# Performance work log

Hardware: AMD Instinct MI355X
Metric: run time of the kernel (lower is better)

The kernel has to match this reference:

```python
import jax, jax.numpy as jnp
import numpy as np

BN_EPS = 1e-5


def setup_inputs() -> dict:
    key = jax.random.key(0)
    ks = jax.random.split(key, 8)
    B, C, H, W = 8, 256, 64, 64
    Cqk = C // 8  # query/key channels = out_channels // 8
    x = jax.random.normal(ks[0], (B, C, H, W), dtype=jnp.float32)
    # 1x1 convs == per-pixel matmuls; kaiming-normal-ish scale
    wq = jax.random.normal(ks[1], (Cqk, C), dtype=jnp.float32) * np.sqrt(2.0 / C)
    bq = jnp.zeros((Cqk,), dtype=jnp.float32)
    wk = jax.random.normal(ks[2], (Cqk, C), dtype=jnp.float32) * np.sqrt(2.0 / C)
    bk = jnp.zeros((Cqk,), dtype=jnp.float32)
    wv = jax.random.normal(ks[3], (C, C), dtype=jnp.float32) * np.sqrt(2.0 / C)
    bv = jnp.zeros((C,), dtype=jnp.float32)
    # gamma is initialized to 0 in the original; use a small nonzero value so
    # the attention path actually contributes (and has nontrivial gradients)
    gamma = jnp.full((1,), 0.5, dtype=jnp.float32)
    bn_weight = jnp.ones((C,), dtype=jnp.float32)
    bn_bias = jnp.zeros((C,), dtype=jnp.float32)
    return {"x": x, "wq": wq, "bq": bq, "wk": wk, "bk": bk,
            "wv": wv, "bv": bv, "gamma": gamma,
            "bn_weight": bn_weight, "bn_bias": bn_bias}


def reference(x, wq, bq, wk, bk, wv, bv, gamma, bn_weight, bn_bias):
    B, C, H, W = x.shape
    N = H * W
    xf = x.reshape(B, C, N)  # (B, C, N)
    # 1x1 conv projections as channel matmuls
    q = jnp.einsum('oc,bcn->bno', wq, xf) + bq            # (B, N, Cqk)
    k = jnp.einsum('oc,bcn->bon', wk, xf) + bk[:, None]   # (B, Cqk, N)
    v = jnp.einsum('oc,bcn->bon', wv, xf) + bv[:, None]   # (B, C, N)
    # attention[b, i, j] = softmax_j(q_i . k_j)  -- full N x N matrix
    scores = jnp.einsum('bno,bom->bnm', q, k)             # (B, N, N)
    attn = jax.nn.softmax(scores, axis=2)
    # out[b, c, i] = sum_j v[b, c, j] * attn[b, i, j]
    out = jnp.einsum('bcj,bij->bci', v, attn)             # (B, C, N)
    out = out.reshape(B, C, H, W)
    out = gamma[0] * out + x
    # BatchNorm2d in training mode: batch statistics over (B, H, W)
    mean = jnp.mean(out, axis=(0, 2, 3), keepdims=True)
    var = jnp.var(out, axis=(0, 2, 3), keepdims=True)
    out = (out - mean) * jax.lax.rsqrt(var + BN_EPS)
    out = out * bn_weight[None, :, None, None] + bn_bias[None, :, None, None]
    return jax.nn.relu(out)
```

## Files before the change

### kernel.cpp

```cpp
#include <hip/hip_runtime.h>
#include <stdint.h>

#define B_ 8
#define C_ 256
#define N_ 4096
#define CQK 32
#define VPANEL (C_ * 64)

typedef __attribute__((ext_vector_type(8))) _Float16 f16x8;
typedef __attribute__((ext_vector_type(4))) float f32x4;

__device__ __forceinline__ unsigned short f2bf_rne(float f) {
  unsigned u = __builtin_bit_cast(unsigned, f);
  u += 0x7FFFu + ((u >> 16) & 1u);
  return (unsigned short)(u >> 16);
}

__global__ __launch_bounds__(256) void xpose_kernel(
    const float* __restrict__ x, _Float16* __restrict__ xT)
{
  __shared__ float xs[64 * 129];
  const int t  = threadIdx.x;
  const int blk = blockIdx.x;
  const int nt = blk & 31;
  const int ct = (blk >> 5) & 3;
  const int b  = blk >> 7;
  const int c0 = ct * 64, n0 = nt * 128;

  #pragma unroll
  for (int p = 0; p < 8; ++p) {
    int cc = p * 8 + (t >> 5);
    int nn = (t & 31) * 4;
    float4 v = *(const float4*)(x + ((size_t)(b * C_ + c0 + cc)) * N_ + n0 + nn);
    xs[cc * 129 + nn]     = v.x;
    xs[cc * 129 + nn + 1] = v.y;
    xs[cc * 129 + nn + 2] = v.z;
    xs[cc * 129 + nn + 3] = v.w;
  }
  __syncthreads();
  #pragma unroll
  for (int p = 0; p < 4; ++p) {
    int id = p * 256 + t;
    int cchunk = id & 7, n = id >> 3;
    _Float16 h[8];
    #pragma unroll
    for (int j = 0; j < 8; ++j) h[j] = (_Float16)xs[(cchunk * 8 + j) * 129 + n];
    *(f16x8*)(xT + ((size_t)(b * N_) + n0 + n) * C_ + c0 + cchunk * 8) = *(f16x8*)h;
  }
}

__global__ __launch_bounds__(256) void wconv_kernel(
    const float* __restrict__ wq, const float* __restrict__ wk,
    const float* __restrict__ wv, _Float16* __restrict__ wf)
{
  int idx = blockIdx.x * 256 + threadIdx.x;
  int e = idx * 4;
  int o = e >> 8, c = e & 255;
  const float* src;
  if (o < 32)      src = wq + o * 256 + c;
  else if (o < 64) src = wk + (o - 32) * 256 + c;
  else             src = wv + (o - 64) * 256 + c;
  float4 v = *(const float4*)src;
  _Float16 h[4] = {(_Float16)v.x, (_Float16)v.y, (_Float16)v.z, (_Float16)v.w};
  *(uint2*)(wf + e) = *(uint2*)h;
}

__global__ __launch_bounds__(256, 4) void proj_gemm_kernel(
    const _Float16* __restrict__ xT, const _Float16* __restrict__ wf,
    const float* __restrict__ bq, const float* __restrict__ bk,
    const float* __restrict__ bv,
    _Float16* __restrict__ qf, _Float16* __restrict__ kf,
    _Float16* __restrict__ vout)
{
  const int t = threadIdx.x, lane = t & 63;
  const int w = t >> 6;
  const int l15 = lane & 15, q4 = lane >> 4;
  const int blk = blockIdx.x;
  const int otile = blk % 5;
  const int nt = blk / 5;
  const int b  = nt >> 5;
  const int n0 = (nt & 31) * 128;
  const int o0w = (w & 1) * 32;
  const int n0w = (w >> 1) * 64;

  f32x4 acc[2][4];
  const f32x4 zf = {0.f, 0.f, 0.f, 0.f};
  #pragma unroll
  for (int a = 0; a < 2; ++a)
    #pragma unroll
    for (int bb = 0; bb < 4; ++bb) acc[a][bb] = zf;

  const _Float16* wbase = wf + (size_t)(otile * 64 + o0w) * 256;
  const _Float16* xbase = xT + ((size_t)(b * N_) + n0 + n0w) * C_;

  #pragma unroll
  for (int kc = 0; kc < 8; ++kc) {
    f16x8 af[2], bfr[4];
    #pragma unroll
    for (int ob = 0; ob < 2; ++ob)
      af[ob] = *(const f16x8*)(wbase + (ob * 16 + l15) * 256 + kc * 32 + q4 * 8);
    #pragma unroll
    for (int nb = 0; nb < 4; ++nb)
      bfr[nb] = *(const f16x8*)(xbase + (nb * 16 + l15) * 256 + kc * 32 + q4 * 8);
    #pragma unroll
    for (int ob = 0; ob < 2; ++ob)
      #pragma unroll
      for (int nb = 0; nb < 4; ++nb)
        acc[ob][nb] = __builtin_amdgcn_mfma_f32_16x16x32_f16(af[ob], bfr[nb], acc[ob][nb], 0, 0, 0);
  }

  if (otile == 0) {
    _Float16* dst = (o0w == 0) ? qf : kf;
    const float* bias = (o0w == 0) ? bq : bk;
    const float qsc = (o0w == 0) ? 1.4426950408889634f : 1.0f;
    #pragma unroll
    for (int ob = 0; ob < 2; ++ob) {
      float4 b4 = *(const float4*)(bias + ob * 16 + q4 * 4);
      #pragma unroll
      for (int nb = 0; nb < 4; ++nb) {
        int pixel = n0 + n0w + nb * 16 + l15;
        _Float16 h[4];
        h[0] = (_Float16)((acc[ob][nb][0] + b4.x) * qsc);
        h[1] = (_Float16)((acc[ob][nb][1] + b4.y) * qsc);
        h[2] = (_Float16)((acc[ob][nb][2] + b4.z) * qsc);
        h[3] = (_Float16)((acc[ob][nb][3] + b4.w) * qsc);
        *(uint2*)(dst + ((size_t)(b * N_) + pixel) * CQK + ob * 16 + q4 * 4) = *(uint2*)h;
      }
    }
  } else {
    int cbase = (otile - 1) * 64 + o0w;
    const int panel = (n0 + n0w) >> 6;
    _Float16* vpan = vout + ((size_t)(b * 64 + panel)) * VPANEL;
    #pragma unroll
    for (int ob = 0; ob < 2; ++ob) {
      float4 b4 = *(const float4*)(bv + cbase + ob * 16 + q4 * 4);
      #pragma unroll
      for (int nb = 0; nb < 4; ++nb) {
        int jj = nb * 16 + l15;
        #pragma unroll
        for (int r = 0; r < 4; ++r) {
          int c = cbase + ob * 16 + q4 * 4 + r;
          float bval = (r == 0) ? b4.x : (r == 1) ? b4.y : (r == 2) ? b4.z : b4.w;
          vpan[(size_t)c * 64 + jj] = (_Float16)(acc[ob][nb][r] + bval);
        }
      }
    }
  }
}

#define ATTN_BODY(K, BUF) do { \
   \
  f16x8 kx_[8]; \
  { const _Float16* kp_ = kbase + (size_t)(K) * 128 * CQK; \
    _Pragma("unroll") \
    for (int jb = 0; jb < 8; ++jb) kx_[jb] = *(const f16x8*)(kp_ + jb * 16 * CQK); } \
   \
  f16x8 vx_[16]; \
  { const _Float16* vp_ = vbase + (size_t)(K) * 2 * VPANEL; \
    _Pragma("unroll") \
    for (int ks = 0; ks < 4; ++ks) \
      _Pragma("unroll") \
      for (int cb = 0; cb < 4; ++cb) \
        vx_[ks * 4 + cb] = *(const f16x8*)(vp_ + (ks >> 1) * VPANEL + cb * 1024 + (ks & 1) * 32); } \
   \
  f32x4 sv_[8]; \
  _Pragma("unroll") \
  for (int jb = 0; jb < 8; ++jb) \
    sv_[jb] = __builtin_amdgcn_mfma_f32_16x16x32_f16(kx_[jb], qfr, zf, 0, 0, 0); \
  float lm_ = sv_[0][0]; \
  _Pragma("unroll") \
  for (int jb = 0; jb < 8; ++jb) \
    lm_ = fmaxf(lm_, fmaxf(fmaxf(sv_[jb][0], sv_[jb][1]), fmaxf(sv_[jb][2], sv_[jb][3]))); \
  lm_ = fmaxf(lm_, __shfl_xor(lm_, 16)); \
  lm_ = fmaxf(lm_, __shfl_xor(lm_, 32)); \
  bool upd_ = lm_ > mold + 8.0f; \
  unsigned long long bal_ = __ballot(upd_);      \
  float alpha_ = upd_ ? exp2f(mold - lm_) : 1.0f; \
  if (upd_) mold = lm_; \
  float ts_ = 0.f; \
  { char* pb_ = (char*)Plds + (BUF) * 17408 + (w * 16 + l15) * 272 + q4 * 8; \
    _Pragma("unroll") \
    for (int jb = 0; jb < 8; ++jb) { \
      float p0_ = exp2f(sv_[jb][0] - mold), p1_ = exp2f(sv_[jb][1] - mold); \
      float p2_ = exp2f(sv_[jb][2] - mold), p3_ = exp2f(sv_[jb][3] - mold); \
      ts_ += (p0_ + p1_) + (p2_ + p3_); \
      _Float16 h_[4] = {(_Float16)p0_, (_Float16)p1_, (_Float16)p2_, (_Float16)p3_}; \
      *(uint2*)(pb_ + jb * 32) = *(uint2*)h_; } } \
  if (q4 == 0) alphal[(BUF) * 64 + w * 16 + l15] = alpha_; \
  if (lane == 0) flagw[(BUF) * 4 + w] = (bal_ != 0ull) ? 1 : 0; \
  ts_ += __shfl_xor(ts_, 16); \
  ts_ += __shfl_xor(ts_, 32); \
  lrun = lrun * alpha_ + ts_; \
  asm volatile("s_waitcnt lgkmcnt(0)" ::: "memory"); \
  __builtin_amdgcn_sched_barrier(0); \
  __builtin_amdgcn_s_barrier(); \
  asm volatile("" ::: "memory"); \
   \
  { int4 fl_ = *(const int4*)(flagw + (BUF) * 4); \
    if (fl_.x | fl_.y | fl_.z | fl_.w) { \
      _Pragma("unroll") \
      for (int ib = 0; ib < 4; ++ib) { \
        float av_ = alphal[(BUF) * 64 + ib * 16 + l15]; \
        _Pragma("unroll") \
        for (int cb = 0; cb < 4; ++cb) \
          _Pragma("unroll") \
          for (int r = 0; r < 4; ++r) acc[cb][ib][r] *= av_; } } } \
   \
  __builtin_amdgcn_s_setprio(1); \
  _Pragma("unroll") \
  for (int ks = 0; ks < 4; ++ks) { \
    f16x8 pf_[4]; \
    _Pragma("unroll") \
    for (int ib = 0; ib < 4; ++ib) \
      pf_[ib] = *(const f16x8*)((char*)Plds + (BUF) * 17408 + (ib * 16 + l15) * 272 + ks * 64 + q4 * 16); \
    _Pragma("unroll") \
    for (int cb = 0; cb < 4; ++cb) \
      _Pragma("unroll") \
      for (int ib = 0; ib < 4; ++ib) \
        acc[cb][ib] = __builtin_amdgcn_mfma_f32_16x16x32_f16(vx_[ks * 4 + cb], pf_[ib], acc[cb][ib], 0, 0, 0); \
  } \
  __builtin_amdgcn_s_setprio(0); \
} while (0)

__global__ __launch_bounds__(256, 2) void attn_kernel(
    const float* __restrict__ x, const float* __restrict__ gptr,
    const _Float16* __restrict__ qf, const _Float16* __restrict__ kf,
    const _Float16* __restrict__ vf, unsigned short* __restrict__ yout)
{
  __shared__ __align__(16) char smem[35648];
  _Float16* Plds  = (_Float16*)smem;
  float* alphal = (float*)(smem + 34816);
  int*   flagw  = (int*)(smem + 35328);
  float* lrowl  = (float*)(smem + 35360);

  const int t = threadIdx.x, lane = t & 63;
  const int w = t >> 6;
  const int l15 = lane & 15, q4 = lane >> 4;
  const int b  = blockIdx.x & 7;
  const int it = blockIdx.x >> 3;
  const int i0 = it * 64;
  const float gamma = gptr[0];

  const f16x8 qfr = *(const f16x8*)(qf + ((size_t)(b * N_) + i0 + w * 16 + l15) * CQK + q4 * 8);

  const _Float16* kbase = kf + ((size_t)(b * N_) + l15) * CQK + q4 * 8;
  const _Float16* vbase = vf + (size_t)b * (64 * VPANEL)
                             + ((size_t)(w * 64 + l15)) * 64 + q4 * 8;

  f32x4 acc[4][4];
  const f32x4 zf = {0.f, 0.f, 0.f, 0.f};
  #pragma unroll
  for (int a = 0; a < 4; ++a)
    #pragma unroll
    for (int bb = 0; bb < 4; ++bb) acc[a][bb] = zf;

  float mold = -1e30f, lrun = 0.f;

  #pragma unroll 1
  for (int k = 0; k < 32; k += 2) {
    ATTN_BODY(k, 0);
    ATTN_BODY(k + 1, 1);
  }

  if (q4 == 0) lrowl[w * 16 + l15] = lrun;
  __syncthreads();
  #pragma unroll
  for (int ib = 0; ib < 4; ++ib) {
    float linv = 1.0f / lrowl[ib * 16 + l15];
    int i = i0 + ib * 16 + l15;
    #pragma unroll
    for (int cb = 0; cb < 4; ++cb) {
      #pragma unroll
      for (int r = 0; r < 4; ++r) {
        int c = w * 64 + cb * 16 + q4 * 4 + r;
        size_t off = ((size_t)(b * C_) + c) * N_ + i;
        float o = acc[cb][ib][r] * linv;
        yout[off] = f2bf_rne(fmaf(gamma, o, x[off]));
      }
    }
  }
}

__global__ __launch_bounds__(256) void bnstats_kernel(
    const unsigned short* __restrict__ y, float* __restrict__ meanw, float* __restrict__ rstdw)
{
  const int c = blockIdx.x;
  const int t = threadIdx.x;
  float s1 = 0.f, s2 = 0.f;
  for (int b = 0; b < B_; ++b) {
    const unsigned short* p = y + ((size_t)(b * C_ + c)) * N_;
    #pragma unroll
    for (int r = 0; r < 2; ++r) {
      uint4 u = *(const uint4*)(p + r * 2048 + t * 8);
      unsigned uu[4] = {u.x, u.y, u.z, u.w};
      #pragma unroll
      for (int k = 0; k < 4; ++k) {
        float a = __builtin_bit_cast(float, uu[k] << 16);
        float bb = __builtin_bit_cast(float, uu[k] & 0xFFFF0000u);
        s1 += a + bb;
        s2 += a * a + bb * bb;
      }
    }
  }
  __shared__ float r1[256], r2[256];
  r1[t] = s1; r2[t] = s2;
  __syncthreads();
  for (int s = 128; s > 0; s >>= 1) {
    if (t < s) { r1[t] += r1[t + s]; r2[t] += r2[t + s]; }
    __syncthreads();
  }
  if (t == 0) {
    float mean = r1[0] * (1.0f / 32768.0f);
    float var  = r2[0] * (1.0f / 32768.0f) - mean * mean;
    meanw[c] = mean;
    rstdw[c] = rsqrtf(var + 1e-5f);
  }
}

__global__ __launch_bounds__(256) void bnapply_kernel(
    const unsigned short* __restrict__ y, float* __restrict__ out,
    const float* __restrict__ meanw, const float* __restrict__ rstdw,
    const float* __restrict__ bnw, const float* __restrict__ bnb)
{
  size_t idx = (size_t)blockIdx.x * 256 + threadIdx.x;
  size_t el = idx * 8;
  int c = (int)((el >> 12) & 255);
  float sc = bnw[c] * rstdw[c];
  float sh = fmaf(-meanw[c], sc, bnb[c]);
  uint4 u = *(const uint4*)(y + el);
  unsigned uu[4] = {u.x, u.y, u.z, u.w};
  float4 o0, o1;
  float v[8];
  #pragma unroll
  for (int k = 0; k < 4; ++k) {
    v[2 * k]     = __builtin_bit_cast(float, uu[k] << 16);
    v[2 * k + 1] = __builtin_bit_cast(float, uu[k] & 0xFFFF0000u);
  }
  o0.x = fmaxf(fmaf(v[0], sc, sh), 0.f);
  o0.y = fmaxf(fmaf(v[1], sc, sh), 0.f);
  o0.z = fmaxf(fmaf(v[2], sc, sh), 0.f);
  o0.w = fmaxf(fmaf(v[3], sc, sh), 0.f);
  o1.x = fmaxf(fmaf(v[4], sc, sh), 0.f);
  o1.y = fmaxf(fmaf(v[5], sc, sh), 0.f);
  o1.z = fmaxf(fmaf(v[6], sc, sh), 0.f);
  o1.w = fmaxf(fmaf(v[7], sc, sh), 0.f);
  *(float4*)(out + el) = o0;
  *(float4*)(out + el + 4) = o1;
}

extern "C" void kernel_launch(void* const* d_in, const int* in_sizes, int n_in,
                              void* d_out, int out_size, void* d_ws, size_t ws_size,
                              hipStream_t stream)
{
  const float* x   = (const float*)d_in[0];
  const float* wq  = (const float*)d_in[1];
  const float* bq  = (const float*)d_in[2];
  const float* wk  = (const float*)d_in[3];
  const float* bk  = (const float*)d_in[4];
  const float* wv  = (const float*)d_in[5];
  const float* bv  = (const float*)d_in[6];
  const float* gm  = (const float*)d_in[7];
  const float* bnw = (const float*)d_in[8];
  const float* bnb = (const float*)d_in[9];
  float* out = (float*)d_out;

  _Float16* xT  = (_Float16*)d_out;
  _Float16* vfp = (_Float16*)((char*)d_out + (size_t)B_ * C_ * N_ * 2);

  char* ws = (char*)d_ws;
  _Float16* qf = (_Float16*)(ws);
  _Float16* kf = (_Float16*)(ws + ((size_t)2 << 20));
  unsigned short* yout = (unsigned short*)(ws + ((size_t)4 << 20));
  _Float16* wf = (_Float16*)(ws + ((size_t)21 << 20));
  float* meanw = (float*)(ws + ((size_t)22 << 20));
  float* rstdw = (float*)(ws + ((size_t)22 << 20) + 4096);

  hipLaunchKernelGGL(xpose_kernel, dim3(1024), dim3(256), 0, stream, x, xT);
  hipLaunchKernelGGL(wconv_kernel, dim3(80), dim3(256), 0, stream, wq, wk, wv, wf);
  hipLaunchKernelGGL(proj_gemm_kernel, dim3(1280), dim3(256), 0, stream,
                     xT, wf, bq, bk, bv, qf, kf, vfp);
  hipLaunchKernelGGL(attn_kernel, dim3(512), dim3(256), 0, stream,
                     x, gm, qf, kf, vfp, yout);
  hipLaunchKernelGGL(bnstats_kernel, dim3(256), dim3(256), 0, stream,
                     yout, meanw, rstdw);
  hipLaunchKernelGGL(bnapply_kernel, dim3(4096), dim3(256), 0, stream,
                     yout, out, meanw, rstdw, bnw, bnb);
}
```

Measured before the change: 297.8 us.

## Fuse x transpose/fp16 conversion into projection GEMM via shared memory

Removes the separate transpose kernel that wrote an fp16 transposed copy of x to global memory. Each projection block now loads a 64-pixel tile of x in fp32, transposes and converts it into an LDS panel, then loops over all five output tiles (q/k plus four v tiles) reusing that panel. This avoids a global write and re-read of the transposed activations and one launch, at the cost of fewer blocks (512), lower occupancy from larger LDS use, and a serialized loop over output tiles per block.

New measurement: 288.9 us. 3.0% less time.

```diff
diff --git a/kernel.cpp b/kernel.cpp
--- a/kernel.cpp
+++ b/kernel.cpp
@@ -14,39 +14,6 @@
   unsigned u = __builtin_bit_cast(unsigned, f);
   u += 0x7FFFu + ((u >> 16) & 1u);
   return (unsigned short)(u >> 16);
-}
-
-__global__ __launch_bounds__(256) void xpose_kernel(
-    const float* __restrict__ x, _Float16* __restrict__ xT)
-{
-  __shared__ float xs[64 * 129];
-  const int t  = threadIdx.x;
-  const int blk = blockIdx.x;
-  const int nt = blk & 31;
-  const int ct = (blk >> 5) & 3;
-  const int b  = blk >> 7;
-  const int c0 = ct * 64, n0 = nt * 128;
-
-  #pragma unroll
-  for (int p = 0; p < 8; ++p) {
-    int cc = p * 8 + (t >> 5);
-    int nn = (t & 31) * 4;
-    float4 v = *(const float4*)(x + ((size_t)(b * C_ + c0 + cc)) * N_ + n0 + nn);
-    xs[cc * 129 + nn]     = v.x;
-    xs[cc * 129 + nn + 1] = v.y;
-    xs[cc * 129 + nn + 2] = v.z;
-    xs[cc * 129 + nn + 3] = v.w;
-  }
-  __syncthreads();
-  #pragma unroll
-  for (int p = 0; p < 4; ++p) {
-    int id = p * 256 + t;
-    int cchunk = id & 7, n = id >> 3;
-    _Float16 h[8];
-    #pragma unroll
-    for (int j = 0; j < 8; ++j) h[j] = (_Float16)xs[(cchunk * 8 + j) * 129 + n];
-    *(f16x8*)(xT + ((size_t)(b * N_) + n0 + n) * C_ + c0 + cchunk * 8) = *(f16x8*)h;
-  }
 }
 
 __global__ __launch_bounds__(256) void wconv_kernel(
@@ -65,96 +32,120 @@
   *(uint2*)(wf + e) = *(uint2*)h;
 }
 
-__global__ __launch_bounds__(256, 4) void proj_gemm_kernel(
-    const _Float16* __restrict__ xT, const _Float16* __restrict__ wf,
+__global__ __launch_bounds__(256, 2) void proj_fused_kernel(
+    const float* __restrict__ x, const _Float16* __restrict__ wf,
     const float* __restrict__ bq, const float* __restrict__ bk,
     const float* __restrict__ bv,
     _Float16* __restrict__ qf, _Float16* __restrict__ kf,
     _Float16* __restrict__ vout)
 {
+  __shared__ float xs[64 * 65];
+  __shared__ _Float16 bp[32 * 64 * 8];
+
   const int t = threadIdx.x, lane = t & 63;
   const int w = t >> 6;
   const int l15 = lane & 15, q4 = lane >> 4;
   const int blk = blockIdx.x;
-  const int otile = blk % 5;
-  const int nt = blk / 5;
-  const int b  = nt >> 5;
-  const int n0 = (nt & 31) * 128;
+  const int b  = blk & 7;
+  const int nt = blk >> 3;
+  const int n0 = nt * 64;
   const int o0w = (w & 1) * 32;
-  const int n0w = (w >> 1) * 64;
-
-  f32x4 acc[2][4];
+  const int n0w = (w >> 1) * 32;
+
+  for (int ct = 0; ct < 4; ++ct) {
+    #pragma unroll
+    for (int p = 0; p < 4; ++p) {
+      int cc = p * 16 + (t >> 4);
+      int nn = (t & 15) * 4;
+      float4 v = *(const float4*)(x + ((size_t)(b * C_) + ct * 64 + cc) * N_ + n0 + nn);
+      xs[cc * 65 + nn]     = v.x;
+      xs[cc * 65 + nn + 1] = v.y;
+      xs[cc * 65 + nn + 2] = v.z;
+      xs[cc * 65 + nn + 3] = v.w;
+    }
+    __syncthreads();
+    #pragma unroll
+    for (int h = 0; h < 2; ++h) {
+      int oct = w + h * 4;
+      int n = lane;
+      _Float16 hh[8];
+      #pragma unroll
+      for (int j = 0; j < 8; ++j) hh[j] = (_Float16)xs[(oct * 8 + j) * 65 + n];
+      *(f16x8*)(bp + (((size_t)(ct * 8 + oct)) * 64 + n) * 8) = *(f16x8*)hh;
+    }
+    __syncthreads();
+  }
+
   const f32x4 zf = {0.f, 0.f, 0.f, 0.f};
-  #pragma unroll
-  for (int a = 0; a < 2; ++a)
-    #pragma unroll
-    for (int bb = 0; bb < 4; ++bb) acc[a][bb] = zf;
-
-  const _Float16* wbase = wf + (size_t)(otile * 64 + o0w) * 256;
-  const _Float16* xbase = xT + ((size_t)(b * N_) + n0 + n0w) * C_;
-
-  #pragma unroll
-  for (int kc = 0; kc < 8; ++kc) {
-    f16x8 af[2], bfr[4];
-    #pragma unroll
-    for (int ob = 0; ob < 2; ++ob)
-      af[ob] = *(const f16x8*)(wbase + (ob * 16 + l15) * 256 + kc * 32 + q4 * 8);
-    #pragma unroll
-    for (int nb = 0; nb < 4; ++nb)
-      bfr[nb] = *(const f16x8*)(xbase + (nb * 16 + l15) * 256 + kc * 32 + q4 * 8);
-    #pragma unroll
-    for (int ob = 0; ob < 2; ++ob)
-      #pragma unroll
-      for (int nb = 0; nb < 4; ++nb)
-        acc[ob][nb] = __builtin_amdgcn_mfma_f32_16x16x32_f16(af[ob], bfr[nb], acc[ob][nb], 0, 0, 0);
-  }
-
-  if (otile == 0) {
-    _Float16* dst = (o0w == 0) ? qf : kf;
-    const float* bias = (o0w == 0) ? bq : bk;
-    const float qsc = (o0w == 0) ? 1.4426950408889634f : 1.0f;
-    #pragma unroll
-    for (int ob = 0; ob < 2; ++ob) {
-      float4 b4 = *(const float4*)(bias + ob * 16 + q4 * 4);
-      #pragma unroll
-      for (int nb = 0; nb < 4; ++nb) {
-        int pixel = n0 + n0w + nb * 16 + l15;
-        _Float16 h[4];
-        h[0] = (_Float16)((acc[ob][nb][0] + b4.x) * qsc);
-        h[1] = (_Float16)((acc[ob][nb][1] + b4.y) * qsc);
-        h[2] = (_Float16)((acc[ob][nb][2] + b4.z) * qsc);
-        h[3] = (_Float16)((acc[ob][nb][3] + b4.w) * qsc);
-        *(uint2*)(dst + ((size_t)(b * N_) + pixel) * CQK + ob * 16 + q4 * 4) = *(uint2*)h;
-      }
-    }
-  } else {
-    int cbase = (otile - 1) * 64 + o0w;
-    const int panel = (n0 + n0w) >> 6;
-    _Float16* vpan = vout + ((size_t)(b * 64 + panel)) * VPANEL;
-    #pragma unroll
-    for (int ob = 0; ob < 2; ++ob) {
-      float4 b4 = *(const float4*)(bv + cbase + ob * 16 + q4 * 4);
-      #pragma unroll
-      for (int nb = 0; nb < 4; ++nb) {
-        int jj = nb * 16 + l15;
+  for (int otile = 0; otile < 5; ++otile) {
+    f32x4 acc[2][2];
+    #pragma unroll
+    for (int a = 0; a < 2; ++a)
+      #pragma unroll
+      for (int bb = 0; bb < 2; ++bb) acc[a][bb] = zf;
+
+    const _Float16* wbase = wf + (size_t)(otile * 64 + o0w) * 256;
+
+    #pragma unroll
+    for (int kc = 0; kc < 8; ++kc) {
+      f16x8 af[2], bfr[2];
+      #pragma unroll
+      for (int ob = 0; ob < 2; ++ob)
+        af[ob] = *(const f16x8*)(wbase + (ob * 16 + l15) * 256 + kc * 32 + q4 * 8);
+      #pragma unroll
+      for (int nb = 0; nb < 2; ++nb)
+        bfr[nb] = *(const f16x8*)(bp + (((size_t)(kc * 4 + q4)) * 64 + n0w + nb * 16 + l15) * 8);
+      #pragma unroll
+      for (int ob = 0; ob < 2; ++ob)
         #pragma unroll
-        for (int r = 0; r < 4; ++r) {
-          int c = cbase + ob * 16 + q4 * 4 + r;
-          float bval = (r == 0) ? b4.x : (r == 1) ? b4.y : (r == 2) ? b4.z : b4.w;
-          vpan[(size_t)c * 64 + jj] = (_Float16)(acc[ob][nb][r] + bval);
+        for (int nb = 0; nb < 2; ++nb)
+          acc[ob][nb] = __builtin_amdgcn_mfma_f32_16x16x32_f16(af[ob], bfr[nb], acc[ob][nb], 0, 0, 0);
+    }
+
+    if (otile == 0) {
+      _Float16* dst = (o0w == 0) ? qf : kf;
+      const float* bias = (o0w == 0) ? bq : bk;
+      const float qsc = (o0w == 0) ? 1.4426950408889634f : 1.0f;
+      #pragma unroll
+      for (int ob = 0; ob < 2; ++ob) {
+        float4 b4 = *(const float4*)(bias + ob * 16 + q4 * 4);
+        #pragma unroll
+        for (int nb = 0; nb < 2; ++nb) {
+          int pixel = n0 + n0w + nb * 16 + l15;
+          _Float16 h[4];
+          h[0] = (_Float16)((acc[ob][nb][0] + b4.x) * qsc);
+          h[1] = (_Float16)((acc[ob][nb][1] + b4.y) * qsc);
+          h[2] = (_Float16)((acc[ob][nb][2] + b4.z) * qsc);
+          h[3] = (_Float16)((acc[ob][nb][3] + b4.w) * qsc);
+          *(uint2*)(dst + ((size_t)(b * N_) + pixel) * CQK + ob * 16 + q4 * 4) = *(uint2*)h;
         }
       }
+    } else {
+      int cbase = (otile - 1) * 64 + o0w;
+      _Float16* vpan = vout + ((size_t)(b * 64 + nt)) * VPANEL;
+      #pragma unroll
+      for (int ob = 0; ob < 2; ++ob) {
+        float4 b4 = *(const float4*)(bv + cbase + ob * 16 + q4 * 4);
+        #pragma unroll
+        for (int nb = 0; nb < 2; ++nb) {
+          int jj = n0w + nb * 16 + l15;
+          #pragma unroll
+          for (int r = 0; r < 4; ++r) {
+            int c = cbase + ob * 16 + q4 * 4 + r;
+            float bval = (r == 0) ? b4.x : (r == 1) ? b4.y : (r == 2) ? b4.z : b4.w;
+            vpan[(size_t)c * 64 + jj] = (_Float16)(acc[ob][nb][r] + bval);
+          }
+        }
+      }
     }
   }
 }
 
 #define ATTN_BODY(K, BUF) do { \
-   \
   f16x8 kx_[8]; \
   { const _Float16* kp_ = kbase + (size_t)(K) * 128 * CQK; \
     _Pragma("unroll") \
     for (int jb = 0; jb < 8; ++jb) kx_[jb] = *(const f16x8*)(kp_ + jb * 16 * CQK); } \
-   \
   f16x8 vx_[16]; \
   { const _Float16* vp_ = vbase + (size_t)(K) * 2 * VPANEL; \
     _Pragma("unroll") \
@@ -162,7 +153,6 @@
       _Pragma("unroll") \
       for (int cb = 0; cb < 4; ++cb) \
         vx_[ks * 4 + cb] = *(const f16x8*)(vp_ + (ks >> 1) * VPANEL + cb * 1024 + (ks & 1) * 32); } \
-   \
   f32x4 sv_[8]; \
   _Pragma("unroll") \
   for (int jb = 0; jb < 8; ++jb) \
@@ -195,7 +185,6 @@
   __builtin_amdgcn_sched_barrier(0); \
   __builtin_amdgcn_s_barrier(); \
   asm volatile("" ::: "memory"); \
-   \
   { int4 fl_ = *(const int4*)(flagw + (BUF) * 4); \
     if (fl_.x | fl_.y | fl_.z | fl_.w) { \
       _Pragma("unroll") \
@@ -205,7 +194,6 @@
         for (int cb = 0; cb < 4; ++cb) \
           _Pragma("unroll") \
           for (int r = 0; r < 4; ++r) acc[cb][ib][r] *= av_; } } } \
-   \
   __builtin_amdgcn_s_setprio(1); \
   _Pragma("unroll") \
   for (int ks = 0; ks < 4; ++ks) { \
@@ -364,7 +352,6 @@
   const float* bnb = (const float*)d_in[9];
   float* out = (float*)d_out;
 
-  _Float16* xT  = (_Float16*)d_out;
   _Float16* vfp = (_Float16*)((char*)d_out + (size_t)B_ * C_ * N_ * 2);
 
   char* ws = (char*)d_ws;
@@ -375,10 +362,9 @@
   float* meanw = (float*)(ws + ((size_t)22 << 20));
   float* rstdw = (float*)(ws + ((size_t)22 << 20) + 4096);
 
-  hipLaunchKernelGGL(xpose_kernel, dim3(1024), dim3(256), 0, stream, x, xT);
   hipLaunchKernelGGL(wconv_kernel, dim3(80), dim3(256), 0, stream, wq, wk, wv, wf);
-  hipLaunchKernelGGL(proj_gemm_kernel, dim3(1280), dim3(256), 0, stream,
-                     xT, wf, bq, bk, bv, qf, kf, vfp);
+  hipLaunchKernelGGL(proj_fused_kernel, dim3(512), dim3(256), 0, stream,
+                     x, wf, bq, bk, bv, qf, kf, vfp);
   hipLaunchKernelGGL(attn_kernel, dim3(512), dim3(256), 0, stream,
                      x, gm, qf, kf, vfp, yout);
   hipLaunchKernelGGL(bnstats_kernel, dim3(256), dim3(256), 0, stream,
```
